# Optimization experiments

Measured on AMD Instinct MI355X. Metric: run time of the kernel, lower is better.

## Reference

```python
import jax, jax.numpy as jnp
import numpy as np

N = 512          # number of ROI boxes
C = 1024         # detector box_head feature dim (in_feats)
HID_REPN = 256   # RePN hidden
HID = 256        # GAT hidden per head
HEADS = 4
NUM_CLASSES = 91
IMG_H, IMG_W = 800.0, 800.0
NEG_SLOPE = 0.2  # PyG GATConv default leaky relu slope


def setup_inputs() -> dict:
    key = jax.random.key(0)
    ks = jax.random.split(key, 12)
    s = 0.05
    feats = jax.random.normal(ks[0], (N, C), jnp.float32)
    # valid boxes: x1<x2, y1<y2, inside 800x800 image
    xy = jax.random.uniform(ks[1], (N, 2), jnp.float32, 0.0, 600.0)
    wh = jax.random.uniform(ks[2], (N, 2), jnp.float32, 10.0, 200.0)
    boxes = jnp.concatenate([xy, xy + wh], axis=1)
    # RelationProposalNetwork params (fc1: [hid, 2C+4], fc2: [1, hid])
    repn_w1 = jax.random.normal(ks[3], (HID_REPN, 2 * C + 4), jnp.float32) * s
    repn_b1 = jnp.zeros((HID_REPN,), jnp.float32)
    repn_w2 = jax.random.normal(ks[4], (1, HID_REPN), jnp.float32) * s
    repn_b2 = jnp.zeros((1,), jnp.float32)
    # AttentionalGCN: GATConv1 (in=C+4 -> HID, HEADS, concat), GATConv2 (HEADS*HID -> NUM_CLASSES, 1 head)
    gat1_w = jax.random.normal(ks[5], (C + 4, HEADS * HID), jnp.float32) * s
    gat1_asrc = jax.random.normal(ks[6], (HEADS, HID), jnp.float32) * s
    gat1_adst = jax.random.normal(ks[7], (HEADS, HID), jnp.float32) * s
    gat1_b = jnp.zeros((HEADS * HID,), jnp.float32)
    gat2_w = jax.random.normal(ks[8], (HEADS * HID, NUM_CLASSES), jnp.float32) * s
    gat2_asrc = jax.random.normal(ks[9], (1, NUM_CLASSES), jnp.float32) * s
    gat2_adst = jax.random.normal(ks[10], (1, NUM_CLASSES), jnp.float32) * s
    gat2_b = jnp.zeros((NUM_CLASSES,), jnp.float32)
    return dict(feats=feats, boxes=boxes,
                repn_w1=repn_w1, repn_b1=repn_b1, repn_w2=repn_w2, repn_b2=repn_b2,
                gat1_w=gat1_w, gat1_asrc=gat1_asrc, gat1_adst=gat1_adst, gat1_b=gat1_b,
                gat2_w=gat2_w, gat2_asrc=gat2_asrc, gat2_adst=gat2_adst, gat2_b=gat2_b,
                k=5)


def _gat_conv(x, src, dst, W, a_src, a_dst, bias, n, heads, out_c, concat_heads):
    # PyG GATConv: h = xW, e_uv = leakyrelu(a_src.h_u + a_dst.h_v), softmax over incoming
    # edges of target v, out_v = sum_u alpha_uv h_u (+ bias). Self-loops already in src/dst.
    h = (x @ W).reshape(n, heads, out_c)                       # [N,H,F]
    a_s = jnp.einsum('nhf,hf->nh', h, a_src)                   # [N,H]
    a_d = jnp.einsum('nhf,hf->nh', h, a_dst)
    e = jax.nn.leaky_relu(a_s[src] + a_d[dst], NEG_SLOPE)      # [E,H]
    m = jax.ops.segment_max(e, dst, num_segments=n)            # [N,H]
    m = jnp.where(jnp.isfinite(m), m, 0.0)
    ex = jnp.exp(e - m[dst])
    denom = jax.ops.segment_sum(ex, dst, num_segments=n)
    alpha = ex / (denom[dst] + 1e-16)                          # [E,H]
    out = jax.ops.segment_sum(alpha[:, :, None] * h[src], dst, num_segments=n)  # [N,H,F]
    out = out.reshape(n, heads * out_c) if concat_heads else out.mean(axis=1)
    return out + bias


def reference(feats, boxes, repn_w1, repn_b1, repn_w2, repn_b2,
              gat1_w, gat1_asrc, gat1_adst, gat1_b,
              gat2_w, gat2_asrc, gat2_adst, gat2_b, k):
    n, c = feats.shape
    # --- RelationProposalNetwork: fc1(cat[f_i, f_j, |b_i-b_j|]) without materializing [N,N,2C+4]
    wf1, wf2, wg = repn_w1[:, :c], repn_w1[:, c:2 * c], repn_w1[:, 2 * c:]
    p1 = feats @ wf1.T                                          # [N,hid]
    p2 = feats @ wf2.T                                          # [N,hid]
    geom_pair = jnp.abs(boxes[:, None, :] - boxes[None, :, :])  # [N,N,4]
    pg = jnp.einsum('ijd,hd->ijh', geom_pair, wg)               # [N,N,hid]
    h = jax.nn.relu(p1[:, None, :] + p2[None, :, :] + pg + repn_b1)
    rel = jnp.einsum('ijh,h->ij', h, repn_w2[0]) + repn_b2[0]   # [N,N] relation scores
    # --- kNN graph via topk (skip self at rank 0), as in _make_edge_index (N > k branch)
    _, idx = jax.lax.top_k(rel, k + 1)
    nbrs = idx[:, 1:]                                           # [N,k]
    src = jnp.repeat(jnp.arange(n), k)
    dst = nbrs.reshape(-1)
    loop = jnp.arange(n)                                        # PyG GATConv adds self-loops
    src = jnp.concatenate([src, loop])
    dst = jnp.concatenate([dst, loop])
    # --- node features: [roi_feats, normalized box geometry]
    scale = jnp.array([IMG_W, IMG_H, IMG_W, IMG_H], jnp.float32)
    nb = boxes / scale
    geom = jnp.stack([nb[:, 0], nb[:, 1], nb[:, 2] - nb[:, 0], nb[:, 3] - nb[:, 1]], axis=1)
    x = jnp.concatenate([feats, geom], axis=1)                  # [N, C+4]
    # --- AttentionalGCN: relu(GAT1) -> GAT2
    h1 = jax.nn.relu(_gat_conv(x, src, dst, gat1_w, gat1_asrc, gat1_adst, gat1_b, n, HEADS, HID, True))
    logits = _gat_conv(h1, src, dst, gat2_w, gat2_asrc, gat2_adst, gat2_b, n, 1, NUM_CLASSES, True)
    probs = jax.nn.softmax(logits, axis=1)                      # per-node class probs
    return logits, probs, rel
```

## Files before the change

### kernel.cpp

```cpp
#include <hip/hip_runtime.h>

#define NCLS 91
#define W1_LD 2052

typedef __attribute__((ext_vector_type(8))) short short8;
typedef __attribute__((ext_vector_type(4))) float f32x4;

__device__ inline ushort bf16_rne(float x) {
    unsigned u = __float_as_uint(x);
    return (ushort)((u + 0x7fffu + ((u >> 16) & 1u)) >> 16);
}

__global__ __launch_bounds__(128) void k_p12(const float* __restrict__ feats,
                                             const float* __restrict__ w1f,
                                             float* __restrict__ pp) {
    int r0 = blockIdx.x * 64, i0 = blockIdx.y * 32, z = blockIdx.z;
    int tid = threadIdx.x, tx = tid & 15, ty = tid >> 4;
    __shared__ float As[64 * 32];
    __shared__ float Bs[64 * 64];
    float* pout = pp + z * 262144;
    int ai = tid & 31, akq = (tid >> 5) * 16;
    int br = tid & 63, bkq = (tid >> 6) * 32;
    const float* abase = feats + (i0 + ai) * 1024 + z * 128 + akq;
    int rg = r0 + br;
    const float* bbase = w1f + (rg < 256 ? rg * W1_LD : (rg - 256) * W1_LD + 1024)
                       + z * 128 + bkq;
    float4 av[4], bv[8];
#pragma unroll
    for (int s = 0; s < 4; ++s) av[s] = *(const float4*)(abase + 4 * s);
#pragma unroll
    for (int s = 0; s < 8; ++s) bv[s] = *(const float4*)(bbase + 4 * s);
    float acc[4][4] = {};
    for (int kt = 0; kt < 2; ++kt) {
#pragma unroll
        for (int s = 0; s < 4; ++s) {
            int k = akq + 4 * s;
            As[(k + 0) * 32 + ai] = av[s].x; As[(k + 1) * 32 + ai] = av[s].y;
            As[(k + 2) * 32 + ai] = av[s].z; As[(k + 3) * 32 + ai] = av[s].w;
        }
#pragma unroll
        for (int s = 0; s < 8; ++s) {
            int k = bkq + 4 * s;
            Bs[(k + 0) * 64 + br] = bv[s].x; Bs[(k + 1) * 64 + br] = bv[s].y;
            Bs[(k + 2) * 64 + br] = bv[s].z; Bs[(k + 3) * 64 + br] = bv[s].w;
        }
        __syncthreads();
        if (kt + 1 < 2) {
#pragma unroll
            for (int s = 0; s < 4; ++s) av[s] = *(const float4*)(abase + 64 + 4 * s);
#pragma unroll
            for (int s = 0; s < 8; ++s) bv[s] = *(const float4*)(bbase + 64 + 4 * s);
        }
#pragma unroll
        for (int k = 0; k < 64; ++k) {
            float4 a4 = *(const float4*)(As + k * 32 + ty * 4);
            float4 b4 = *(const float4*)(Bs + k * 64 + tx * 4);
            acc[0][0] = fmaf(a4.x, b4.x, acc[0][0]); acc[0][1] = fmaf(a4.x, b4.y, acc[0][1]);
            acc[0][2] = fmaf(a4.x, b4.z, acc[0][2]); acc[0][3] = fmaf(a4.x, b4.w, acc[0][3]);
            acc[1][0] = fmaf(a4.y, b4.x, acc[1][0]); acc[1][1] = fmaf(a4.y, b4.y, acc[1][1]);
            acc[1][2] = fmaf(a4.y, b4.z, acc[1][2]); acc[1][3] = fmaf(a4.y, b4.w, acc[1][3]);
            acc[2][0] = fmaf(a4.z, b4.x, acc[2][0]); acc[2][1] = fmaf(a4.z, b4.y, acc[2][1]);
            acc[2][2] = fmaf(a4.z, b4.z, acc[2][2]); acc[2][3] = fmaf(a4.z, b4.w, acc[2][3]);
            acc[3][0] = fmaf(a4.w, b4.x, acc[3][0]); acc[3][1] = fmaf(a4.w, b4.y, acc[3][1]);
            acc[3][2] = fmaf(a4.w, b4.z, acc[3][2]); acc[3][3] = fmaf(a4.w, b4.w, acc[3][3]);
        }
        __syncthreads();
    }
#pragma unroll
    for (int ii = 0; ii < 4; ++ii)
        *(float4*)(pout + (i0 + ty * 4 + ii) * 512 + r0 + tx * 4) =
            make_float4(acc[ii][0], acc[ii][1], acc[ii][2], acc[ii][3]);
}

__global__ __launch_bounds__(256) void k_psum(const float* __restrict__ pp,
                                              float* __restrict__ ppsum) {
    int idx = (blockIdx.x * 256 + threadIdx.x) * 4;
    float4 a = *(const float4*)(pp + idx);
#pragma unroll
    for (int p = 1; p < 8; ++p) {
        float4 v = *(const float4*)(pp + p * 262144 + idx);
        a.x += v.x; a.y += v.y; a.z += v.z; a.w += v.w;
    }
    *(float4*)(ppsum + idx) = a;
}

__global__ __launch_bounds__(256) void k_rel(const float* __restrict__ ppsum,
                                             const float* __restrict__ w1f,
                                             const float* __restrict__ b1f,
                                             const float* __restrict__ w2f,
                                             const float* __restrict__ boxesf,
                                             float* __restrict__ r0,
                                             float* __restrict__ prel) {
    int j0 = blockIdx.x * 64, i0 = blockIdx.y * 16, z = blockIdx.z;
    int tid = threadIdx.x, tx = tid & 63, ty = tid >> 6;
    __shared__ float As1[32 * 17];
    __shared__ float Bs[32 * 64];
    __shared__ float Awg[32 * 4];
    __shared__ float Aw2[32];
    float4 bj = *(const float4*)(boxesf + (j0 + tx) * 4);
    float g[4][4];
#pragma unroll
    for (int s = 0; s < 4; ++s) {
        float4 bi = *(const float4*)(boxesf + (i0 + ty * 4 + s) * 4);
        g[s][0] = fabsf(bi.x - bj.x); g[s][1] = fabsf(bi.y - bj.y);
        g[s][2] = fabsf(bi.z - bj.z); g[s][3] = fabsf(bi.w - bj.w);
    }
    float acc[4] = {0.f, 0.f, 0.f, 0.f};
    int ali = tid & 15, alh = (tid >> 4) * 4;
    int blj = tid & 63, blh = (tid >> 6) * 8;
    for (int c4 = 0; c4 < 2; ++c4) {
        int hb = (z * 2 + c4) * 32;
        if (tid < 128) {
            float4 a4 = *(const float4*)(ppsum + (i0 + ali) * 512 + hb + alh);
            float4 b  = *(const float4*)(b1f + hb + alh);
            As1[(alh + 0) * 17 + ali] = a4.x + b.x;
            As1[(alh + 1) * 17 + ali] = a4.y + b.y;
            As1[(alh + 2) * 17 + ali] = a4.z + b.z;
            As1[(alh + 3) * 17 + ali] = a4.w + b.w;
        }
#pragma unroll
        for (int s = 0; s < 2; ++s) {
            int h = blh + 4 * s;
            float4 u4 = *(const float4*)(ppsum + (j0 + blj) * 512 + 256 + hb + h);
            Bs[(h + 0) * 64 + blj] = u4.x;
            Bs[(h + 1) * 64 + blj] = u4.y;
            Bs[(h + 2) * 64 + blj] = u4.z;
            Bs[(h + 3) * 64 + blj] = u4.w;
        }
        if (tid < 32) {
            int hg = hb + tid;
            *(float4*)(Awg + tid * 4) = *(const float4*)(w1f + hg * W1_LD + 2048);
            Aw2[tid] = w2f[hg];
        }
        __syncthreads();
#pragma unroll
        for (int hh = 0; hh < 32; ++hh) {
            float4 wg = *(const float4*)(Awg + hh * 4);
            float w2v = Aw2[hh];
            float p2v = Bs[hh * 64 + tx];
            float s0 = As1[hh * 17 + ty * 4 + 0];
            float s1 = As1[hh * 17 + ty * 4 + 1];
            float s2 = As1[hh * 17 + ty * 4 + 2];
            float s3 = As1[hh * 17 + ty * 4 + 3];
            float t0 = s0 + p2v;
            t0 = fmaf(g[0][0], wg.x, t0); t0 = fmaf(g[0][1], wg.y, t0);
            t0 = fmaf(g[0][2], wg.z, t0); t0 = fmaf(g[0][3], wg.w, t0);
            acc[0] = fmaf(w2v, fmaxf(t0, 0.f), acc[0]);
            float t1 = s1 + p2v;
            t1 = fmaf(g[1][0], wg.x, t1); t1 = fmaf(g[1][1], wg.y, t1);
            t1 = fmaf(g[1][2], wg.z, t1); t1 = fmaf(g[1][3], wg.w, t1);
            acc[1] = fmaf(w2v, fmaxf(t1, 0.f), acc[1]);
            float t2 = s2 + p2v;
            t2 = fmaf(g[2][0], wg.x, t2); t2 = fmaf(g[2][1], wg.y, t2);
            t2 = fmaf(g[2][2], wg.z, t2); t2 = fmaf(g[2][3], wg.w, t2);
            acc[2] = fmaf(w2v, fmaxf(t2, 0.f), acc[2]);
            float t3 = s3 + p2v;
            t3 = fmaf(g[3][0], wg.x, t3); t3 = fmaf(g[3][1], wg.y, t3);
            t3 = fmaf(g[3][2], wg.z, t3); t3 = fmaf(g[3][3], wg.w, t3);
            acc[3] = fmaf(w2v, fmaxf(t3, 0.f), acc[3]);
        }
        __syncthreads();
    }
    float* po = (z == 0) ? r0 : (prel + (z - 1) * 262144);
#pragma unroll
    for (int s = 0; s < 4; ++s)
        po[(i0 + ty * 4 + s) * 512 + j0 + tx] = acc[s];
}

__global__ void k_topk(const float* __restrict__ r0, const float* __restrict__ prel,
                       const float* __restrict__ b2f, const int* __restrict__ kp,
                       int* __restrict__ nbrs, int* __restrict__ count,
                       float* __restrict__ rel_out) {
    int i = blockIdx.x, lane = threadIdx.x;
    int k = *kp;
    float b2v = b2f[0];
    float v[8]; int ids[8];
    for (int q = 0; q < 8; ++q) {
        int j = lane + 64 * q;
        float val = r0[i * 512 + j] + prel[i * 512 + j]
                  + prel[262144 + i * 512 + j] + prel[524288 + i * 512 + j] + b2v;
        rel_out[i * 512 + j] = val;
        v[q] = val;
        ids[q] = j;
    }
    for (int pick = 0; pick < k + 1; ++pick) {
        float bv = -INFINITY; int bidx = 1 << 30;
        for (int q = 0; q < 8; ++q)
            if (v[q] > bv || (v[q] == bv && ids[q] < bidx)) { bv = v[q]; bidx = ids[q]; }
        for (int off = 32; off > 0; off >>= 1) {
            float ov = __shfl_down(bv, off);
            int oi = __shfl_down(bidx, off);
            if (ov > bv || (ov == bv && oi < bidx)) { bv = ov; bidx = oi; }
        }
        bv = __shfl(bv, 0); bidx = __shfl(bidx, 0);
        if (pick >= 1 && lane == 0) {
            nbrs[i * 8 + (pick - 1)] = bidx;
            atomicAdd(&count[bidx], 1);
        }
        for (int q = 0; q < 8; ++q) if (ids[q] == bidx) v[q] = -INFINITY;
    }
    if (lane == 0) atomicAdd(&count[i], 1);
}

__global__ void k_scanfill(const int* __restrict__ count, const int* __restrict__ nbrs,
                           const int* __restrict__ kp,
                           int* __restrict__ offs, int* __restrict__ inlist) {
    __shared__ int s[512];
    __shared__ int excl[512];
    __shared__ int cur[512];
    int t = threadIdx.x;
    int c = count[t];
    s[t] = c; cur[t] = 0;
    __syncthreads();
    for (int off = 1; off < 512; off <<= 1) {
        int v = (t >= off) ? s[t - off] : 0;
        __syncthreads();
        s[t] += v;
        __syncthreads();
    }
    offs[t + 1] = s[t];
    if (t == 0) offs[0] = 0;
    excl[t] = s[t] - c;
    __syncthreads();
    int k = *kp;
    for (int q = 0; q < k; ++q) {
        int d = nbrs[t * 8 + q] & 511;
        int pos = atomicAdd(&cur[d], 1);
        inlist[excl[d] + pos] = t;
    }
    int pos = atomicAdd(&cur[t], 1);
    inlist[excl[t] + pos] = t;
}

__global__ __launch_bounds__(256) void k_conv(const float* __restrict__ feats,
                                              const float* __restrict__ Wg,
                                              ushort* __restrict__ Afh,
                                              ushort* __restrict__ Afl,
                                              ushort* __restrict__ Bfh,
                                              ushort* __restrict__ Bfl,
                                              int* __restrict__ zero_ints) {
    int b = blockIdx.x, t = threadIdx.x;
    if (b < 2) zero_ints[b * 256 + t] = 0;
    int lane = t & 63;
    float x[8];
    size_t off;
    if (b < 256) {
        int g = b * 256 + t;
        int q = g >> 6;
        int it = q & 31, kt = q >> 5;
        int row = it * 16 + (lane & 15);
        int col0 = kt * 32 + (lane >> 4) * 8;
        const float* src = feats + row * 1024 + col0;
        float4 u0 = *(const float4*)(src);
        float4 u1 = *(const float4*)(src + 4);
        x[0] = u0.x; x[1] = u0.y; x[2] = u0.z; x[3] = u0.w;
        x[4] = u1.x; x[5] = u1.y; x[6] = u1.z; x[7] = u1.w;
        off = ((size_t)(kt * 32 + it) * 64 + lane) * 8;
    } else {
        int g = (b - 256) * 256 + t;
        int q = g >> 6;
        int nt = q & 63, kt = q >> 6;
        int col = nt * 16 + (lane & 15);
        int row0 = kt * 32 + (lane >> 4) * 8;
#pragma unroll
        for (int e = 0; e < 8; ++e) x[e] = Wg[(row0 + e) * 1024 + col];
        off = ((size_t)(kt * 64 + nt) * 64 + lane) * 8;
        Afh = Bfh; Afl = Bfl;
    }
    uint uh[4], ul[4];
#pragma unroll
    for (int p = 0; p < 4; ++p) {
        ushort h0 = bf16_rne(x[2 * p]);
        ushort h1 = bf16_rne(x[2 * p + 1]);
        float f0 = __uint_as_float((unsigned)h0 << 16);
        float f1 = __uint_as_float((unsigned)h1 << 16);
        ushort l0 = bf16_rne(x[2 * p] - f0);
        ushort l1 = bf16_rne(x[2 * p + 1] - f1);
        uh[p] = (uint)h0 | ((uint)h1 << 16);
        ul[p] = (uint)l0 | ((uint)l1 << 16);
    }
    *(uint4*)(Afh + off) = make_uint4(uh[0], uh[1], uh[2], uh[3]);
    *(uint4*)(Afl + off) = make_uint4(ul[0], ul[1], ul[2], ul[3]);
}

__global__ __launch_bounds__(256) void k_mm1(const ushort* __restrict__ Afh,
                                             const ushort* __restrict__ Afl,
                                             const ushort* __restrict__ Bfh,
                                             const ushort* __restrict__ Bfl,
                                             float* __restrict__ P) {
    int nt0 = blockIdx.x * 4, it0 = blockIdx.y * 4, z = blockIdx.z;
    int t = threadIdx.x, lane = t & 63, w = t >> 6;
    int wr = w >> 1, wc = w & 1, sub = w;
    __shared__ uint4 buf[2][4][4][64];
    const uint4* gAh = (const uint4*)Afh;
    const uint4* gAl = (const uint4*)Afl;
    const uint4* gBh = (const uint4*)Bfh;
    const uint4* gBl = (const uint4*)Bfl;
    f32x4 acc[2][2];
    f32x4 zero = {0.f, 0.f, 0.f, 0.f};
    acc[0][0] = zero; acc[0][1] = zero; acc[1][0] = zero; acc[1][1] = zero;
    int ktg = z * 8;
    uint4 rah = gAh[(ktg * 32 + it0 + sub) * 64 + lane];
    uint4 ral = gAl[(ktg * 32 + it0 + sub) * 64 + lane];
    uint4 rbh = gBh[(ktg * 64 + nt0 + sub) * 64 + lane];
    uint4 rbl = gBl[(ktg * 64 + nt0 + sub) * 64 + lane];
    for (int kk = 0; kk < 8; ++kk) {
        int cur = kk & 1;
        buf[cur][0][sub][lane] = rah;
        buf[cur][1][sub][lane] = ral;
        buf[cur][2][sub][lane] = rbh;
        buf[cur][3][sub][lane] = rbl;
        __syncthreads();
        if (kk < 7) {
            int kn = ktg + kk + 1;
            rah = gAh[(kn * 32 + it0 + sub) * 64 + lane];
            ral = gAl[(kn * 32 + it0 + sub) * 64 + lane];
            rbh = gBh[(kn * 64 + nt0 + sub) * 64 + lane];
            rbl = gBl[(kn * 64 + nt0 + sub) * 64 + lane];
        }
        short8 ah[2], al[2], bh[2], bl[2];
#pragma unroll
        for (int i = 0; i < 2; ++i) {
            ah[i] = *(const short8*)&buf[cur][0][2 * wr + i][lane];
            al[i] = *(const short8*)&buf[cur][1][2 * wr + i][lane];
            bh[i] = *(const short8*)&buf[cur][2][2 * wc + i][lane];
            bl[i] = *(const short8*)&buf[cur][3][2 * wc + i][lane];
        }
#pragma unroll
        for (int i = 0; i < 2; ++i)
#pragma unroll
            for (int j = 0; j < 2; ++j) {
                acc[i][j] = __builtin_amdgcn_mfma_f32_16x16x32_bf16(ah[i], bh[j], acc[i][j], 0, 0, 0);
                acc[i][j] = __builtin_amdgcn_mfma_f32_16x16x32_bf16(ah[i], bl[j], acc[i][j], 0, 0, 0);
                acc[i][j] = __builtin_amdgcn_mfma_f32_16x16x32_bf16(al[i], bh[j], acc[i][j], 0, 0, 0);
            }
        __syncthreads();
    }
    float* outp = P + z * 524288;
#pragma unroll
    for (int i = 0; i < 2; ++i)
#pragma unroll
        for (int j = 0; j < 2; ++j) {
            int rbase = (it0 + 2 * wr + i) * 16 + (lane >> 4) * 4;
            int c = (nt0 + 2 * wc + j) * 16 + (lane & 15);
#pragma unroll
            for (int r = 0; r < 4; ++r)
                outp[(size_t)(rbase + r) * 1024 + c] = acc[i][j][r];
        }
}

__global__ __launch_bounds__(256) void k_gat1ep(const float* __restrict__ P,
                                                const float* __restrict__ boxesf,
                                                const float* __restrict__ Wg,
                                                const float* __restrict__ asrcf,
                                                const float* __restrict__ adstf,
                                                float* __restrict__ hX,
                                                float* __restrict__ a_s1,
                                                float* __restrict__ a_d1) {
    int i = blockIdx.x, t = threadIdx.x;
    const float* P0 = P;
    const float* P1 = P + 524288;
    const float* P2 = P + 1048576;
    const float* P3 = P + 1572864;
    float4 bx = *(const float4*)(boxesf + i * 4);
    float g0 = bx.x / 800.f, g1 = bx.y / 800.f;
    float g2 = bx.z / 800.f - g0, g3 = bx.w / 800.f - g1;
    float ps[4], pd[4];
#pragma unroll
    for (int q = 0; q < 4; ++q) {
        int c = q * 256 + t;
        float v = P0[i * 1024 + c] + P1[i * 1024 + c] + P2[i * 1024 + c] + P3[i * 1024 + c];
        v = fmaf(g0, Wg[1024 * 1024 + c], v);
        v = fmaf(g1, Wg[1025 * 1024 + c], v);
        v = fmaf(g2, Wg[1026 * 1024 + c], v);
        v = fmaf(g3, Wg[1027 * 1024 + c], v);
        hX[i * 1024 + c] = v;
        ps[q] = v * asrcf[c];
        pd[q] = v * adstf[c];
    }
    __shared__ float rs[4][4], rd[4][4];
    int wid = t >> 6;
#pragma unroll
    for (int off = 32; off > 0; off >>= 1) {
#pragma unroll
        for (int q = 0; q < 4; ++q) {
            ps[q] += __shfl_down(ps[q], off);
            pd[q] += __shfl_down(pd[q], off);
        }
    }
    if ((t & 63) == 0) {
#pragma unroll
        for (int q = 0; q < 4; ++q) { rs[wid][q] = ps[q]; rd[wid][q] = pd[q]; }
    }
    __syncthreads();
    if (t < 4)
        a_s1[i * 4 + t] = rs[0][t] + rs[1][t] + rs[2][t] + rs[3][t];
    else if (t < 8) {
        int q = t - 4;
        a_d1[i * 4 + q] = rd[0][q] + rd[1][q] + rd[2][q] + rd[3][q];
    }
}

__global__ void k_aggr1(const float* __restrict__ hX,
                        const float* __restrict__ a_s, const float* __restrict__ a_d,
                        const int* __restrict__ offs, const int* __restrict__ inlist,
                        const float* __restrict__ bias,
                        float* __restrict__ h1) {
    int n = blockIdx.x, t = threadIdx.x;
    int beg = offs[n], deg = offs[n + 1] - beg;
    if (deg > 513) deg = 513;
    __shared__ int srcs[520];
    __shared__ float alpha[520][4];
    __shared__ float sm[4];
    for (int e = t; e < deg; e += 256) srcs[e] = inlist[beg + e] & 511;
    __syncthreads();
    for (int idx = t; idx < deg * 4; idx += 256) {
        int e = idx >> 2, q = idx & 3;
        float sc = a_s[srcs[e] * 4 + q] + a_d[n * 4 + q];
        alpha[e][q] = (sc >= 0.f) ? sc : 0.2f * sc;
    }
    __syncthreads();
    if (t < 4) {
        float m = -INFINITY;
        for (int e = 0; e < deg; ++e) m = fmaxf(m, alpha[e][t]);
        if (!isfinite(m)) m = 0.f;
        float s = 0.f;
        for (int e = 0; e < deg; ++e) { float ex = expf(alpha[e][t] - m); alpha[e][t] = ex; s += ex; }
        sm[t] = s + 1e-16f;
    }
    __syncthreads();
    for (int idx = t; idx < deg * 4; idx += 256) {
        int e = idx >> 2, q = idx & 3;
        alpha[e][q] /= sm[q];
    }
    __syncthreads();
    for (int q = 0; q < 4; ++q) {
        float acc = 0.f;
        for (int e = 0; e < deg; ++e) acc += alpha[e][q] * hX[srcs[e] * 1024 + q * 256 + t];
        h1[n * 1024 + q * 256 + t] = fmaxf(acc + bias[q * 256 + t], 0.f);
    }
}

__global__ __launch_bounds__(256) void k_gat2(const float* __restrict__ h1,
                                              const float* __restrict__ Wf,
                                              const float* __restrict__ asrcf,
                                              const float* __restrict__ adstf,
                                              float* __restrict__ h2,
                                              float* __restrict__ a_s2,
                                              float* __restrict__ a_d2) {
    int n = blockIdx.x, t = threadIdx.x;
    __shared__ float xs[1024];
    __shared__ float hbuf[NCLS];
    __shared__ float sred[256], dred[256];
    for (int c = t; c < 1024; c += 256) xs[c] = h1[n * 1024 + c];
    __syncthreads();
    int cls = t & 127, kh = t >> 7;
    float acc = 0.f;
    if (cls < NCLS) {
        const float* wp = Wf + (kh * 512) * NCLS + cls;
        const float* xp = xs + kh * 512;
        float a0 = 0.f, a1 = 0.f, a2 = 0.f, a3 = 0.f;
        for (int c = 0; c < 512; c += 4) {
            a0 = fmaf(xp[c + 0], wp[(c + 0) * NCLS], a0);
            a1 = fmaf(xp[c + 1], wp[(c + 1) * NCLS], a1);
            a2 = fmaf(xp[c + 2], wp[(c + 2) * NCLS], a2);
            a3 = fmaf(xp[c + 3], wp[(c + 3) * NCLS], a3);
        }
        acc = (a0 + a1) + (a2 + a3);
    }
    if (kh == 0 && cls < NCLS) hbuf[cls] = acc;
    __syncthreads();
    float tot = 0.f;
    int act = (kh == 1 && cls < NCLS);
    if (act) { tot = acc + hbuf[cls]; h2[n * NCLS + cls] = tot; }
    sred[t] = act ? tot * asrcf[cls] : 0.f;
    dred[t] = act ? tot * adstf[cls] : 0.f;
    __syncthreads();
    for (int s = 128; s > 0; s >>= 1) {
        if (t < s) { sred[t] += sred[t + s]; dred[t] += dred[t + s]; }
        __syncthreads();
    }
    if (t == 0) { a_s2[n] = sred[0]; a_d2[n] = dred[0]; }
}

__global__ void k_aggr2(const float* __restrict__ h2,
                        const float* __restrict__ a_s2, const float* __restrict__ a_d2,
                        const int* __restrict__ offs, const int* __restrict__ inlist,
                        const float* __restrict__ bias,
                        float* __restrict__ logits_out,
                        float* __restrict__ probs_out) {
    int n = blockIdx.x, t = threadIdx.x;
    int beg = offs[n], deg = offs[n + 1] - beg;
    if (deg > 513) deg = 513;
    __shared__ int srcs[520];
    __shared__ float alpha[520];
    __shared__ float red[128];
    __shared__ float smden;
    for (int e = t; e < deg; e += 128) {
        int s = inlist[beg + e] & 511;
        srcs[e] = s;
        float sc = a_s2[s] + a_d2[n];
        alpha[e] = (sc >= 0.f) ? sc : 0.2f * sc;
    }
    __syncthreads();
    if (t == 0) {
        float m = -INFINITY;
        for (int e = 0; e < deg; ++e) m = fmaxf(m, alpha[e]);
        if (!isfinite(m)) m = 0.f;
        float s = 0.f;
        for (int e = 0; e < deg; ++e) { float ex = expf(alpha[e] - m); alpha[e] = ex; s += ex; }
        smden = s + 1e-16f;
    }
    __syncthreads();
    float logit = 0.f;
    if (t < NCLS) {
        float acc = 0.f;
        for (int e = 0; e < deg; ++e) acc += alpha[e] * h2[srcs[e] * NCLS + t];
        logit = acc / smden + bias[t];
        logits_out[n * NCLS + t] = logit;
    }
    red[t] = (t < NCLS) ? logit : -INFINITY; __syncthreads();
    for (int s = 64; s > 0; s >>= 1) { if (t < s) red[t] = fmaxf(red[t], red[t + s]); __syncthreads(); }
    float mx = red[0];
    __syncthreads();
    float ex = (t < NCLS) ? expf(logit - mx) : 0.f;
    red[t] = ex; __syncthreads();
    for (int s = 64; s > 0; s >>= 1) { if (t < s) red[t] += red[t + s]; __syncthreads(); }
    float inv = 1.f / red[0];
    if (t < NCLS) probs_out[n * NCLS + t] = ex * inv;
}

extern "C" void kernel_launch(void* const* d_in, const int* in_sizes, int n_in,
                              void* d_out, int out_size, void* d_ws, size_t ws_size,
                              hipStream_t stream) {
    const float* feats   = (const float*)d_in[0];
    const float* boxes   = (const float*)d_in[1];
    const float* repn_w1 = (const float*)d_in[2];
    const float* repn_b1 = (const float*)d_in[3];
    const float* repn_w2 = (const float*)d_in[4];
    const float* repn_b2 = (const float*)d_in[5];
    const float* gat1_w    = (const float*)d_in[6];
    const float* gat1_asrc = (const float*)d_in[7];
    const float* gat1_adst = (const float*)d_in[8];
    const float* gat1_b    = (const float*)d_in[9];
    const float* gat2_w    = (const float*)d_in[10];
    const float* gat2_asrc = (const float*)d_in[11];
    const float* gat2_adst = (const float*)d_in[12];
    const float* gat2_b    = (const float*)d_in[13];
    const int* kp = (const int*)d_in[14];

    float* out = (float*)d_out;
    float* logits_out = out;
    float* probs_out  = out + 512 * NCLS;
    float* rel_out    = out + 2 * 512 * NCLS;

    float* wsf   = (float*)d_ws;
    float* pp    = wsf;
    float* P     = wsf;
    float* hX    = P;
    float* h1    = P + 524288;
    float* ppsum = wsf + 2097152;
    float* prel  = wsf + 2359296;
    ushort* Afh  = (ushort*)(wsf + 3145728);
    ushort* Afl  = (ushort*)(wsf + 3407872);
    ushort* Bfh  = (ushort*)(wsf + 3670016);
    ushort* Bfl  = (ushort*)(wsf + 4194304);
    float* h2    = wsf + 4718592;
    float* a_s2  = wsf + 4765696;
    float* a_d2  = wsf + 4766208;
    float* a_s1  = wsf + 4766720;
    float* a_d1  = wsf + 4768768;
    int* ib      = (int*)(wsf + 4770816);
    int* count   = ib;
    int* nbrs    = ib + 1024;
    int* offs    = ib + 5120;
    int* inlist  = ib + 5640;

    k_conv<<<dim3(768), dim3(256), 0, stream>>>(feats, gat1_w, Afh, Afl, Bfh, Bfl, ib);
    k_p12<<<dim3(8, 16, 8), dim3(128), 0, stream>>>(feats, repn_w1, pp);
    k_psum<<<dim3(256), dim3(256), 0, stream>>>(pp, ppsum);
    k_rel<<<dim3(8, 32, 4), dim3(256), 0, stream>>>(ppsum, repn_w1, repn_b1, repn_w2,
                                                    boxes, rel_out, prel);
    k_topk<<<dim3(512), dim3(64), 0, stream>>>(rel_out, prel, repn_b2, kp,
                                               nbrs, count, rel_out);
    k_scanfill<<<dim3(1), dim3(512), 0, stream>>>(count, nbrs, kp, offs, inlist);
    k_mm1<<<dim3(16, 8, 4), dim3(256), 0, stream>>>(Afh, Afl, Bfh, Bfl, P);
    k_gat1ep<<<dim3(512), dim3(256), 0, stream>>>(P, boxes, gat1_w, gat1_asrc,
                                                  gat1_adst, hX, a_s1, a_d1);
    k_aggr1<<<dim3(512), dim3(256), 0, stream>>>(hX, a_s1, a_d1, offs, inlist, gat1_b, h1);
    k_gat2<<<dim3(512), dim3(256), 0, stream>>>(h1, gat2_w, gat2_asrc, gat2_adst,
                                                h2, a_s2, a_d2);
    k_aggr2<<<dim3(512), dim3(128), 0, stream>>>(h2, a_s2, a_d2, offs, inlist, gat2_b,
                                                 logits_out, probs_out);
}
```

Measured before the change: 186.0 us.

## Merge independent kernels via block-range dispatch to cut launch count

Independent stages are combined into shared launches by splitting on block index. The bf16 conversion now runs inside the RePN partial GEMM launch, the GAT1 MFMA GEMM inside the relation-score launch, and the scan/fill inside the GAT1 epilogue as an extra block. This removes three kernel launches and their serialization gaps and lets independent work overlap on the GPU. The cost is larger shared-memory unions, heterogeneous blocks that may hurt occupancy, and a single-block scan now sharing a launch with 512 other blocks.

```diff
diff --git a/kernel.cpp b/kernel.cpp
--- a/kernel.cpp
+++ b/kernel.cpp
@@ -11,13 +11,67 @@
     return (ushort)((u + 0x7fffu + ((u >> 16) & 1u)) >> 16);
 }
 
-__global__ __launch_bounds__(128) void k_p12(const float* __restrict__ feats,
+__global__ __launch_bounds__(128) void k_pre(const float* __restrict__ feats,
+                                             const float* __restrict__ Wg,
+                                             ushort* __restrict__ Afh,
+                                             ushort* __restrict__ Afl,
+                                             ushort* __restrict__ Bfh,
+                                             ushort* __restrict__ Bfl,
+                                             int* __restrict__ zero_ints,
                                              const float* __restrict__ w1f,
                                              float* __restrict__ pp) {
-    int r0 = blockIdx.x * 64, i0 = blockIdx.y * 32, z = blockIdx.z;
-    int tid = threadIdx.x, tx = tid & 15, ty = tid >> 4;
+    int b = blockIdx.x, tid = threadIdx.x;
     __shared__ float As[64 * 32];
     __shared__ float Bs[64 * 64];
+    if (b < 1536) {
+        if (b < 4) zero_ints[b * 128 + tid] = 0;
+        int lane = tid & 63;
+        float x[8];
+        size_t off;
+        ushort *oh, *ol;
+        if (b < 512) {
+            int g = b * 128 + tid;
+            int q = g >> 6;
+            int it = q & 31, kt = q >> 5;
+            int row = it * 16 + (lane & 15);
+            int col0 = kt * 32 + (lane >> 4) * 8;
+            const float* src = feats + row * 1024 + col0;
+            float4 u0 = *(const float4*)(src);
+            float4 u1 = *(const float4*)(src + 4);
+            x[0] = u0.x; x[1] = u0.y; x[2] = u0.z; x[3] = u0.w;
+            x[4] = u1.x; x[5] = u1.y; x[6] = u1.z; x[7] = u1.w;
+            off = ((size_t)(kt * 32 + it) * 64 + lane) * 8;
+            oh = Afh; ol = Afl;
+        } else {
+            int g = (b - 512) * 128 + tid;
+            int q = g >> 6;
+            int nt = q & 63, kt = q >> 6;
+            int col = nt * 16 + (lane & 15);
+            int row0 = kt * 32 + (lane >> 4) * 8;
+#pragma unroll
+            for (int e = 0; e < 8; ++e) x[e] = Wg[(row0 + e) * 1024 + col];
+            off = ((size_t)(kt * 64 + nt) * 64 + lane) * 8;
+            oh = Bfh; ol = Bfl;
+        }
+        uint uh[4], ul[4];
+#pragma unroll
+        for (int p = 0; p < 4; ++p) {
+            ushort h0 = bf16_rne(x[2 * p]);
+            ushort h1 = bf16_rne(x[2 * p + 1]);
+            float f0 = __uint_as_float((unsigned)h0 << 16);
+            float f1 = __uint_as_float((unsigned)h1 << 16);
+            ushort l0 = bf16_rne(x[2 * p] - f0);
+            ushort l1 = bf16_rne(x[2 * p + 1] - f1);
+            uh[p] = (uint)h0 | ((uint)h1 << 16);
+            ul[p] = (uint)l0 | ((uint)l1 << 16);
+        }
+        *(uint4*)(oh + off) = make_uint4(uh[0], uh[1], uh[2], uh[3]);
+        *(uint4*)(ol + off) = make_uint4(ul[0], ul[1], ul[2], ul[3]);
+        return;
+    }
+    int bx = b - 1536;
+    int r0 = (bx & 7) * 64, i0 = ((bx >> 3) & 15) * 32, z = bx >> 7;
+    int tx = tid & 15, ty = tid >> 4;
     float* pout = pp + z * 262144;
     int ai = tid & 31, akq = (tid >> 5) * 16;
     int br = tid & 63, bkq = (tid >> 6) * 32;
@@ -84,87 +138,159 @@
     *(float4*)(ppsum + idx) = a;
 }
 
-__global__ __launch_bounds__(256) void k_rel(const float* __restrict__ ppsum,
-                                             const float* __restrict__ w1f,
-                                             const float* __restrict__ b1f,
-                                             const float* __restrict__ w2f,
-                                             const float* __restrict__ boxesf,
-                                             float* __restrict__ r0,
-                                             float* __restrict__ prel) {
-    int j0 = blockIdx.x * 64, i0 = blockIdx.y * 16, z = blockIdx.z;
-    int tid = threadIdx.x, tx = tid & 63, ty = tid >> 6;
-    __shared__ float As1[32 * 17];
-    __shared__ float Bs[32 * 64];
-    __shared__ float Awg[32 * 4];
-    __shared__ float Aw2[32];
-    float4 bj = *(const float4*)(boxesf + (j0 + tx) * 4);
-    float g[4][4];
-#pragma unroll
-    for (int s = 0; s < 4; ++s) {
-        float4 bi = *(const float4*)(boxesf + (i0 + ty * 4 + s) * 4);
-        g[s][0] = fabsf(bi.x - bj.x); g[s][1] = fabsf(bi.y - bj.y);
-        g[s][2] = fabsf(bi.z - bj.z); g[s][3] = fabsf(bi.w - bj.w);
-    }
-    float acc[4] = {0.f, 0.f, 0.f, 0.f};
-    int ali = tid & 15, alh = (tid >> 4) * 4;
-    int blj = tid & 63, blh = (tid >> 6) * 8;
-    for (int c4 = 0; c4 < 2; ++c4) {
-        int hb = (z * 2 + c4) * 32;
-        if (tid < 128) {
-            float4 a4 = *(const float4*)(ppsum + (i0 + ali) * 512 + hb + alh);
-            float4 b  = *(const float4*)(b1f + hb + alh);
-            As1[(alh + 0) * 17 + ali] = a4.x + b.x;
-            As1[(alh + 1) * 17 + ali] = a4.y + b.y;
-            As1[(alh + 2) * 17 + ali] = a4.z + b.z;
-            As1[(alh + 3) * 17 + ali] = a4.w + b.w;
-        }
-#pragma unroll
-        for (int s = 0; s < 2; ++s) {
-            int h = blh + 4 * s;
-            float4 u4 = *(const float4*)(ppsum + (j0 + blj) * 512 + 256 + hb + h);
-            Bs[(h + 0) * 64 + blj] = u4.x;
-            Bs[(h + 1) * 64 + blj] = u4.y;
-            Bs[(h + 2) * 64 + blj] = u4.z;
-            Bs[(h + 3) * 64 + blj] = u4.w;
-        }
-        if (tid < 32) {
-            int hg = hb + tid;
-            *(float4*)(Awg + tid * 4) = *(const float4*)(w1f + hg * W1_LD + 2048);
-            Aw2[tid] = w2f[hg];
-        }
+__global__ __launch_bounds__(256) void k_relmm(const float* __restrict__ ppsum,
+                                               const float* __restrict__ w1f,
+                                               const float* __restrict__ b1f,
+                                               const float* __restrict__ w2f,
+                                               const float* __restrict__ boxesf,
+                                               float* __restrict__ r0,
+                                               float* __restrict__ prel,
+                                               const ushort* __restrict__ Afh,
+                                               const ushort* __restrict__ Afl,
+                                               const ushort* __restrict__ Bfh,
+                                               const ushort* __restrict__ Bfl,
+                                               float* __restrict__ P) {
+    __shared__ union SM {
+        struct { float As1[32 * 17]; float Bs[32 * 64]; float Awg[32 * 4]; float Aw2[32]; } r;
+        uint4 buf[2][4][4][64];
+    } sm;
+    int b = blockIdx.x;
+    if (b < 1024) {
+        int j0 = (b & 7) * 64, i0 = ((b >> 3) & 31) * 16, z = b >> 8;
+        int tid = threadIdx.x, tx = tid & 63, ty = tid >> 6;
+        float* As1 = sm.r.As1;
+        float* Bs  = sm.r.Bs;
+        float* Awg = sm.r.Awg;
+        float* Aw2 = sm.r.Aw2;
+        float4 bj = *(const float4*)(boxesf + (j0 + tx) * 4);
+        float g[4][4];
+#pragma unroll
+        for (int s = 0; s < 4; ++s) {
+            float4 bi = *(const float4*)(boxesf + (i0 + ty * 4 + s) * 4);
+            g[s][0] = fabsf(bi.x - bj.x); g[s][1] = fabsf(bi.y - bj.y);
+            g[s][2] = fabsf(bi.z - bj.z); g[s][3] = fabsf(bi.w - bj.w);
+        }
+        float acc[4] = {0.f, 0.f, 0.f, 0.f};
+        int ali = tid & 15, alh = (tid >> 4) * 4;
+        int blj = tid & 63, blh = (tid >> 6) * 8;
+        for (int c4 = 0; c4 < 2; ++c4) {
+            int hb = (z * 2 + c4) * 32;
+            if (tid < 128) {
+                float4 a4 = *(const float4*)(ppsum + (i0 + ali) * 512 + hb + alh);
+                float4 bb = *(const float4*)(b1f + hb + alh);
+                As1[(alh + 0) * 17 + ali] = a4.x + bb.x;
+                As1[(alh + 1) * 17 + ali] = a4.y + bb.y;
+                As1[(alh + 2) * 17 + ali] = a4.z + bb.z;
+                As1[(alh + 3) * 17 + ali] = a4.w + bb.w;
+            }
+#pragma unroll
+            for (int s = 0; s < 2; ++s) {
+                int h = blh + 4 * s;
+                float4 u4 = *(const float4*)(ppsum + (j0 + blj) * 512 + 256 + hb + h);
+                Bs[(h + 0) * 64 + blj] = u4.x;
+                Bs[(h + 1) * 64 + blj] = u4.y;
+                Bs[(h + 2) * 64 + blj] = u4.z;
+                Bs[(h + 3) * 64 + blj] = u4.w;
+            }
+            if (tid < 32) {
+                int hg = hb + tid;
+                *(float4*)(Awg + tid * 4) = *(const float4*)(w1f + hg * W1_LD + 2048);
+                Aw2[tid] = w2f[hg];
+            }
+            __syncthreads();
+#pragma unroll
+            for (int hh = 0; hh < 32; ++hh) {
+                float4 wg = *(const float4*)(Awg + hh * 4);
+                float w2v = Aw2[hh];
+                float p2v = Bs[hh * 64 + tx];
+                float s0 = As1[hh * 17 + ty * 4 + 0];
+                float s1 = As1[hh * 17 + ty * 4 + 1];
+                float s2 = As1[hh * 17 + ty * 4 + 2];
+                float s3 = As1[hh * 17 + ty * 4 + 3];
+                float t0 = s0 + p2v;
+                t0 = fmaf(g[0][0], wg.x, t0); t0 = fmaf(g[0][1], wg.y, t0);
+                t0 = fmaf(g[0][2], wg.z, t0); t0 = fmaf(g[0][3], wg.w, t0);
+                acc[0] = fmaf(w2v, fmaxf(t0, 0.f), acc[0]);
+                float t1 = s1 + p2v;
+                t1 = fmaf(g[1][0], wg.x, t1); t1 = fmaf(g[1][1], wg.y, t1);
+                t1 = fmaf(g[1][2], wg.z, t1); t1 = fmaf(g[1][3], wg.w, t1);
+                acc[1] = fmaf(w2v, fmaxf(t1, 0.f), acc[1]);
+                float t2 = s2 + p2v;
+                t2 = fmaf(g[2][0], wg.x, t2); t2 = fmaf(g[2][1], wg.y, t2);
+                t2 = fmaf(g[2][2], wg.z, t2); t2 = fmaf(g[2][3], wg.w, t2);
+                acc[2] = fmaf(w2v, fmaxf(t2, 0.f), acc[2]);
+                float t3 = s3 + p2v;
+                t3 = fmaf(g[3][0], wg.x, t3); t3 = fmaf(g[3][1], wg.y, t3);
+                t3 = fmaf(g[3][2], wg.z, t3); t3 = fmaf(g[3][3], wg.w, t3);
+                acc[3] = fmaf(w2v, fmaxf(t3, 0.f), acc[3]);
+            }
+            __syncthreads();
+        }
+        float* po = (z == 0) ? r0 : (prel + (z - 1) * 262144);
+#pragma unroll
+        for (int s = 0; s < 4; ++s)
+            po[(i0 + ty * 4 + s) * 512 + j0 + tx] = acc[s];
+        return;
+    }
+    int m = b - 1024;
+    int nt0 = (m & 15) * 4, it0 = ((m >> 4) & 7) * 4, z = m >> 7;
+    int t = threadIdx.x, lane = t & 63, w = t >> 6;
+    int wr = w >> 1, wc = w & 1, sub = w;
+    const uint4* gAh = (const uint4*)Afh;
+    const uint4* gAl = (const uint4*)Afl;
+    const uint4* gBh = (const uint4*)Bfh;
+    const uint4* gBl = (const uint4*)Bfl;
+    f32x4 acc[2][2];
+    f32x4 zero = {0.f, 0.f, 0.f, 0.f};
+    acc[0][0] = zero; acc[0][1] = zero; acc[1][0] = zero; acc[1][1] = zero;
+    int ktg = z * 8;
+    uint4 rah = gAh[(ktg * 32 + it0 + sub) * 64 + lane];
+    uint4 ral = gAl[(ktg * 32 + it0 + sub) * 64 + lane];
+    uint4 rbh = gBh[(ktg * 64 + nt0 + sub) * 64 + lane];
+    uint4 rbl = gBl[(ktg * 64 + nt0 + sub) * 64 + lane];
+    for (int kk = 0; kk < 8; ++kk) {
+        int cur = kk & 1;
+        sm.buf[cur][0][sub][lane] = rah;
+        sm.buf[cur][1][sub][lane] = ral;
+        sm.buf[cur][2][sub][lane] = rbh;
+        sm.buf[cur][3][sub][lane] = rbl;
         __syncthreads();
-#pragma unroll
-        for (int hh = 0; hh < 32; ++hh) {
-            float4 wg = *(const float4*)(Awg + hh * 4);
-            float w2v = Aw2[hh];
-            float p2v = Bs[hh * 64 + tx];
-            float s0 = As1[hh * 17 + ty * 4 + 0];
-            float s1 = As1[hh * 17 + ty * 4 + 1];
-            float s2 = As1[hh * 17 + ty * 4 + 2];
-            float s3 = As1[hh * 17 + ty * 4 + 3];
-            float t0 = s0 + p2v;
-            t0 = fmaf(g[0][0], wg.x, t0); t0 = fmaf(g[0][1], wg.y, t0);
-            t0 = fmaf(g[0][2], wg.z, t0); t0 = fmaf(g[0][3], wg.w, t0);
-            acc[0] = fmaf(w2v, fmaxf(t0, 0.f), acc[0]);
-            float t1 = s1 + p2v;
-            t1 = fmaf(g[1][0], wg.x, t1); t1 = fmaf(g[1][1], wg.y, t1);
-            t1 = fmaf(g[1][2], wg.z, t1); t1 = fmaf(g[1][3], wg.w, t1);
-            acc[1] = fmaf(w2v, fmaxf(t1, 0.f), acc[1]);
-            float t2 = s2 + p2v;
-            t2 = fmaf(g[2][0], wg.x, t2); t2 = fmaf(g[2][1], wg.y, t2);
-            t2 = fmaf(g[2][2], wg.z, t2); t2 = fmaf(g[2][3], wg.w, t2);
-            acc[2] = fmaf(w2v, fmaxf(t2, 0.f), acc[2]);
-            float t3 = s3 + p2v;
-            t3 = fmaf(g[3][0], wg.x, t3); t3 = fmaf(g[3][1], wg.y, t3);
-            t3 = fmaf(g[3][2], wg.z, t3); t3 = fmaf(g[3][3], wg.w, t3);
-            acc[3] = fmaf(w2v, fmaxf(t3, 0.f), acc[3]);
-        }
+        if (kk < 7) {
+            int kn = ktg + kk + 1;
+            rah = gAh[(kn * 32 + it0 + sub) * 64 + lane];
+            ral = gAl[(kn * 32 + it0 + sub) * 64 + lane];
+            rbh = gBh[(kn * 64 + nt0 + sub) * 64 + lane];
+            rbl = gBl[(kn * 64 + nt0 + sub) * 64 + lane];
+        }
+        short8 ah[2], al[2], bh[2], bl[2];
+#pragma unroll
+        for (int i = 0; i < 2; ++i) {
+            ah[i] = *(const short8*)&sm.buf[cur][0][2 * wr + i][lane];
+            al[i] = *(const short8*)&sm.buf[cur][1][2 * wr + i][lane];
+            bh[i] = *(const short8*)&sm.buf[cur][2][2 * wc + i][lane];
+            bl[i] = *(const short8*)&sm.buf[cur][3][2 * wc + i][lane];
+        }
+#pragma unroll
+        for (int i = 0; i < 2; ++i)
+#pragma unroll
+            for (int j = 0; j < 2; ++j) {
+                acc[i][j] = __builtin_amdgcn_mfma_f32_16x16x32_bf16(ah[i], bh[j], acc[i][j], 0, 0, 0);
+                acc[i][j] = __builtin_amdgcn_mfma_f32_16x16x32_bf16(ah[i], bl[j], acc[i][j], 0, 0, 0);
+                acc[i][j] = __builtin_amdgcn_mfma_f32_16x16x32_bf16(al[i], bh[j], acc[i][j], 0, 0, 0);
+            }
         __syncthreads();
     }
-    float* po = (z == 0) ? r0 : (prel + (z - 1) * 262144);
-#pragma unroll
-    for (int s = 0; s < 4; ++s)
-        po[(i0 + ty * 4 + s) * 512 + j0 + tx] = acc[s];
+    float* outp = P + z * 524288;
+#pragma unroll
+    for (int i = 0; i < 2; ++i)
+#pragma unroll
+        for (int j = 0; j < 2; ++j) {
+            int rbase = (it0 + 2 * wr + i) * 16 + (lane >> 4) * 4;
+            int c = (nt0 + 2 * wc + j) * 16 + (lane & 15);
+#pragma unroll
+            for (int r = 0; r < 4; ++r)
+                outp[(size_t)(rbase + r) * 1024 + c] = acc[i][j][r];
+        }
 }
 
 __global__ void k_topk(const float* __restrict__ r0, const float* __restrict__ prel,
@@ -202,162 +328,54 @@
     if (lane == 0) atomicAdd(&count[i], 1);
 }
 
-__global__ void k_scanfill(const int* __restrict__ count, const int* __restrict__ nbrs,
-                           const int* __restrict__ kp,
-                           int* __restrict__ offs, int* __restrict__ inlist) {
-    __shared__ int s[512];
-    __shared__ int excl[512];
-    __shared__ int cur[512];
+__global__ __launch_bounds__(256) void k_epsf(const float* __restrict__ P,
+                                              const float* __restrict__ boxesf,
+                                              const float* __restrict__ Wg,
+                                              const float* __restrict__ asrcf,
+                                              const float* __restrict__ adstf,
+                                              float* __restrict__ hX,
+                                              float* __restrict__ a_s1,
+                                              float* __restrict__ a_d1,
+                                              const int* __restrict__ count,
+                                              const int* __restrict__ nbrs,
+                                              const int* __restrict__ kp,
+                                              int* __restrict__ offs,
+                                              int* __restrict__ inlist) {
+    __shared__ int ss[512], excl[512], cur[512];
+    __shared__ float rs[4][4], rd[4][4];
     int t = threadIdx.x;
-    int c = count[t];
-    s[t] = c; cur[t] = 0;
-    __syncthreads();
-    for (int off = 1; off < 512; off <<= 1) {
-        int v = (t >= off) ? s[t - off] : 0;
+    if (blockIdx.x == 512) {
+        int c0 = count[t], c1 = count[t + 256];
+        ss[t] = c0; ss[t + 256] = c1; cur[t] = 0; cur[t + 256] = 0;
         __syncthreads();
-        s[t] += v;
+        for (int off = 1; off < 512; off <<= 1) {
+            int v0 = (t >= off) ? ss[t - off] : 0;
+            int v1 = (t + 256 >= off) ? ss[t + 256 - off] : 0;
+            __syncthreads();
+            ss[t] += v0; ss[t + 256] += v1;
+            __syncthreads();
+        }
+        offs[t + 1] = ss[t];
+        offs[t + 257] = ss[t + 256];
+        if (t == 0) offs[0] = 0;
+        excl[t] = ss[t] - c0;
+        excl[t + 256] = ss[t + 256] - c1;
         __syncthreads();
-    }
-    offs[t + 1] = s[t];
-    if (t == 0) offs[0] = 0;
-    excl[t] = s[t] - c;
-    __syncthreads();
-    int k = *kp;
-    for (int q = 0; q < k; ++q) {
-        int d = nbrs[t * 8 + q] & 511;
-        int pos = atomicAdd(&cur[d], 1);
-        inlist[excl[d] + pos] = t;
-    }
-    int pos = atomicAdd(&cur[t], 1);
-    inlist[excl[t] + pos] = t;
-}
-
-__global__ __launch_bounds__(256) void k_conv(const float* __restrict__ feats,
-                                              const float* __restrict__ Wg,
-                                              ushort* __restrict__ Afh,
-                                              ushort* __restrict__ Afl,
-                                              ushort* __restrict__ Bfh,
-                                              ushort* __restrict__ Bfl,
-                                              int* __restrict__ zero_ints) {
-    int b = blockIdx.x, t = threadIdx.x;
-    if (b < 2) zero_ints[b * 256 + t] = 0;
-    int lane = t & 63;
-    float x[8];
-    size_t off;
-    if (b < 256) {
-        int g = b * 256 + t;
-        int q = g >> 6;
-        int it = q & 31, kt = q >> 5;
-        int row = it * 16 + (lane & 15);
-        int col0 = kt * 32 + (lane >> 4) * 8;
-        const float* src = feats + row * 1024 + col0;
-        float4 u0 = *(const float4*)(src);
-        float4 u1 = *(const float4*)(src + 4);
-        x[0] = u0.x; x[1] = u0.y; x[2] = u0.z; x[3] = u0.w;
-        x[4] = u1.x; x[5] = u1.y; x[6] = u1.z; x[7] = u1.w;
-        off = ((size_t)(kt * 32 + it) * 64 + lane) * 8;
-    } else {
-        int g = (b - 256) * 256 + t;
-        int q = g >> 6;
-        int nt = q & 63, kt = q >> 6;
-        int col = nt * 16 + (lane & 15);
-        int row0 = kt * 32 + (lane >> 4) * 8;
-#pragma unroll
-        for (int e = 0; e < 8; ++e) x[e] = Wg[(row0 + e) * 1024 + col];
-        off = ((size_t)(kt * 64 + nt) * 64 + lane) * 8;
-        Afh = Bfh; Afl = Bfl;
-    }
-    uint uh[4], ul[4];
-#pragma unroll
-    for (int p = 0; p < 4; ++p) {
-        ushort h0 = bf16_rne(x[2 * p]);
-        ushort h1 = bf16_rne(x[2 * p + 1]);
-        float f0 = __uint_as_float((unsigned)h0 << 16);
-        float f1 = __uint_as_float((unsigned)h1 << 16);
-        ushort l0 = bf16_rne(x[2 * p] - f0);
-        ushort l1 = bf16_rne(x[2 * p + 1] - f1);
-        uh[p] = (uint)h0 | ((uint)h1 << 16);
-        ul[p] = (uint)l0 | ((uint)l1 << 16);
-    }
-    *(uint4*)(Afh + off) = make_uint4(uh[0], uh[1], uh[2], uh[3]);
-    *(uint4*)(Afl + off) = make_uint4(ul[0], ul[1], ul[2], ul[3]);
-}
-
-__global__ __launch_bounds__(256) void k_mm1(const ushort* __restrict__ Afh,
-                                             const ushort* __restrict__ Afl,
-                                             const ushort* __restrict__ Bfh,
-                                             const ushort* __restrict__ Bfl,
-                                             float* __restrict__ P) {
-    int nt0 = blockIdx.x * 4, it0 = blockIdx.y * 4, z = blockIdx.z;
-    int t = threadIdx.x, lane = t & 63, w = t >> 6;
-    int wr = w >> 1, wc = w & 1, sub = w;
-    __shared__ uint4 buf[2][4][4][64];
-    const uint4* gAh = (const uint4*)Afh;
-    const uint4* gAl = (const uint4*)Afl;
-    const uint4* gBh = (const uint4*)Bfh;
-    const uint4* gBl = (const uint4*)Bfl;
-    f32x4 acc[2][2];
-    f32x4 zero = {0.f, 0.f, 0.f, 0.f};
-    acc[0][0] = zero; acc[0][1] = zero; acc[1][0] = zero; acc[1][1] = zero;
-    int ktg = z * 8;
-    uint4 rah = gAh[(ktg * 32 + it0 + sub) * 64 + lane];
-    uint4 ral = gAl[(ktg * 32 + it0 + sub) * 64 + lane];
-    uint4 rbh = gBh[(ktg * 64 + nt0 + sub) * 64 + lane];
-    uint4 rbl = gBl[(ktg * 64 + nt0 + sub) * 64 + lane];
-    for (int kk = 0; kk < 8; ++kk) {
-        int cur = kk & 1;
-        buf[cur][0][sub][lane] = rah;
-        buf[cur][1][sub][lane] = ral;
-        buf[cur][2][sub][lane] = rbh;
-        buf[cur][3][sub][lane] = rbl;
-        __syncthreads();
-        if (kk < 7) {
-            int kn = ktg + kk + 1;
-            rah = gAh[(kn * 32 + it0 + sub) * 64 + lane];
-            ral = gAl[(kn * 32 + it0 + sub) * 64 + lane];
-            rbh = gBh[(kn * 64 + nt0 + sub) * 64 + lane];
-            rbl = gBl[(kn * 64 + nt0 + sub) * 64 + lane];
-        }
-        short8 ah[2], al[2], bh[2], bl[2];
-#pragma unroll
-        for (int i = 0; i < 2; ++i) {
-            ah[i] = *(const short8*)&buf[cur][0][2 * wr + i][lane];
-            al[i] = *(const short8*)&buf[cur][1][2 * wr + i][lane];
-            bh[i] = *(const short8*)&buf[cur][2][2 * wc + i][lane];
-            bl[i] = *(const short8*)&buf[cur][3][2 * wc + i][lane];
-        }
-#pragma unroll
-        for (int i = 0; i < 2; ++i)
-#pragma unroll
-            for (int j = 0; j < 2; ++j) {
-                acc[i][j] = __builtin_amdgcn_mfma_f32_16x16x32_bf16(ah[i], bh[j], acc[i][j], 0, 0, 0);
-                acc[i][j] = __builtin_amdgcn_mfma_f32_16x16x32_bf16(ah[i], bl[j], acc[i][j], 0, 0, 0);
-                acc[i][j] = __builtin_amdgcn_mfma_f32_16x16x32_bf16(al[i], bh[j], acc[i][j], 0, 0, 0);
+        int k = *kp;
+#pragma unroll
+        for (int h = 0; h < 2; ++h) {
+            int node = t + h * 256;
+            for (int q = 0; q < k; ++q) {
+                int d = nbrs[node * 8 + q] & 511;
+                int pos = atomicAdd(&cur[d], 1);
+                inlist[excl[d] + pos] = node;
             }
-        __syncthreads();
-    }
-    float* outp = P + z * 524288;
-#pragma unroll
-    for (int i = 0; i < 2; ++i)
-#pragma unroll
-        for (int j = 0; j < 2; ++j) {
-            int rbase = (it0 + 2 * wr + i) * 16 + (lane >> 4) * 4;
-            int c = (nt0 + 2 * wc + j) * 16 + (lane & 15);
-#pragma unroll
-            for (int r = 0; r < 4; ++r)
-                outp[(size_t)(rbase + r) * 1024 + c] = acc[i][j][r];
-        }
-}
-
-__global__ __launch_bounds__(256) void k_gat1ep(const float* __restrict__ P,
-                                                const float* __restrict__ boxesf,
-                                                const float* __restrict__ Wg,
-                                                const float* __restrict__ asrcf,
-                                                const float* __restrict__ adstf,
-                                                float* __restrict__ hX,
-                                                float* __restrict__ a_s1,
-                                                float* __restrict__ a_d1) {
-    int i = blockIdx.x, t = threadIdx.x;
+            int pos = atomicAdd(&cur[node], 1);
+            inlist[excl[node] + pos] = node;
+        }
+        return;
+    }
+    int i = blockIdx.x;
     const float* P0 = P;
     const float* P1 = P + 524288;
     const float* P2 = P + 1048576;
@@ -378,7 +396,6 @@
         ps[q] = v * asrcf[c];
         pd[q] = v * adstf[c];
     }
-    __shared__ float rs[4][4], rd[4][4];
     int wid = t >> 6;
 #pragma unroll
     for (int off = 32; off > 0; off >>= 1) {
@@ -576,17 +593,17 @@
     int* offs    = ib + 5120;
     int* inlist  = ib + 5640;
 
-    k_conv<<<dim3(768), dim3(256), 0, stream>>>(feats, gat1_w, Afh, Afl, Bfh, Bfl, ib);
-    k_p12<<<dim3(8, 16, 8), dim3(128), 0, stream>>>(feats, repn_w1, pp);
+    k_pre<<<dim3(2560), dim3(128), 0, stream>>>(feats, gat1_w, Afh, Afl, Bfh, Bfl,
+                                                ib, repn_w1, pp);
     k_psum<<<dim3(256), dim3(256), 0, stream>>>(pp, ppsum);
-    k_rel<<<dim3(8, 32, 4), dim3(256), 0, stream>>>(ppsum, repn_w1, repn_b1, repn_w2,
-                                                    boxes, rel_out, prel);
+    k_relmm<<<dim3(1536), dim3(256), 0, stream>>>(ppsum, repn_w1, repn_b1, repn_w2,
+                                                  boxes, rel_out, prel,
+                                                  Afh, Afl, Bfh, Bfl, P);
     k_topk<<<dim3(512), dim3(64), 0, stream>>>(rel_out, prel, repn_b2, kp,
                                                nbrs, count, rel_out);
-    k_scanfill<<<dim3(1), dim3(512), 0, stream>>>(count, nbrs, kp, offs, inlist);
-    k_mm1<<<dim3(16, 8, 4), dim3(256), 0, stream>>>(Afh, Afl, Bfh, Bfl, P);
-    k_gat1ep<<<dim3(512), dim3(256), 0, stream>>>(P, boxes, gat1_w, gat1_asrc,
-                                                  gat1_adst, hX, a_s1, a_d1);
+    k_epsf<<<dim3(513), dim3(256), 0, stream>>>(P, boxes, gat1_w, gat1_asrc, gat1_adst,
+                                                hX, a_s1, a_d1,
+                                                count, nbrs, kp, offs, inlist);
     k_aggr1<<<dim3(512), dim3(256), 0, stream>>>(hX, a_s1, a_d1, offs, inlist, gat1_b, h1);
     k_gat2<<<dim3(512), dim3(256), 0, stream>>>(h1, gat2_w, gat2_asrc, gat2_adst,
                                                 h2, a_s2, a_d2);
```

Measured after the change: 179.0 us. -3.7%, faster.
